# Optimization experiments

Hardware: AMD Instinct MI355X
Metric: run time of the kernel (lower is better)

Reference implementation:

```python
import jax, jax.numpy as jnp
import numpy as np

D_IN = 768
D_OUT = 768
NUM_HEADS = 12
HEAD_DIM = D_OUT // NUM_HEADS
SEQ = 4096
BATCH = 1


def setup_inputs() -> dict:
    key = jax.random.key(0)
    ks = jax.random.split(key, 6)
    s = 1.0 / np.sqrt(D_IN)
    return {
        "x": jax.random.normal(ks[0], (BATCH, SEQ, D_IN), dtype=jnp.float32),
        "W_query": jax.random.normal(ks[1], (D_IN, D_OUT), dtype=jnp.float32) * s,
        "W_key": jax.random.normal(ks[2], (D_IN, D_OUT), dtype=jnp.float32) * s,
        "W_value": jax.random.normal(ks[3], (D_IN, D_OUT), dtype=jnp.float32) * s,
        "W_out": jax.random.normal(ks[4], (D_OUT, D_OUT), dtype=jnp.float32) * s,
        "b_out": jax.random.normal(ks[5], (D_OUT,), dtype=jnp.float32) * 0.01,
    }


def reference(x, W_query, W_key, W_value, W_out, b_out):
    B, S, _ = x.shape
    # QKV projections (qkv_bias=False)
    q = (x @ W_query).reshape(B, S, NUM_HEADS, HEAD_DIM)
    k = (x @ W_key).reshape(B, S, NUM_HEADS, HEAD_DIM)
    v = (x @ W_value).reshape(B, S, NUM_HEADS, HEAD_DIM)
    # attention scores [B, H, S, S] with causal mask
    scores = jnp.einsum("bqhd,bkhd->bhqk", q, k) / jnp.sqrt(
        jnp.asarray(HEAD_DIM, dtype=x.dtype)
    )
    causal = jnp.tril(jnp.ones((S, S), dtype=bool))
    scores = jnp.where(causal, scores, jnp.finfo(x.dtype).min)
    attn = jax.nn.softmax(scores, axis=-1)  # dropout p=0.0 -> identity
    ctx = jnp.einsum("bhqk,bkhd->bqhd", attn, v).reshape(B, S, D_OUT)
    return ctx @ W_out + b_out
```

## Files before the change

### kernel.cpp

```cpp
#include <hip/hip_runtime.h>
#include <stdint.h>

#define SEQ 4096
#define DM 768
#define NH 12
#define HD 64

typedef __attribute__((ext_vector_type(8))) short bf8;
typedef __attribute__((ext_vector_type(4))) float f4;
typedef __attribute__((ext_vector_type(16))) float f32x16;

static __device__ __forceinline__ f4 mfma_bf16(bf8 a, bf8 b, f4 c) {
  return __builtin_amdgcn_mfma_f32_16x16x32_bf16(a, b, c, 0, 0, 0);
}
static __device__ __forceinline__ f32x16 mfma32(bf8 a, bf8 b, f32x16 c) {
  return __builtin_amdgcn_mfma_f32_32x32x16_bf16(a, b, c, 0, 0, 0);
}

static __device__ __forceinline__ unsigned short f2bf(float f) {
  unsigned int u = __float_as_uint(f);
  u += 0x7FFFu + ((u >> 16) & 1u);
  return (unsigned short)(u >> 16);
}

static __device__ __forceinline__ unsigned int cvtpk(float lo, float hi) {
  unsigned int r;
  asm("v_cvt_pk_bf16_f32 %0, %1, %2" : "=v"(r) : "v"(lo), "v"(hi));
  return r;
}

static __device__ __forceinline__ void gload_lds16(const void* g, void* l) {
  __builtin_amdgcn_global_load_lds(
      (const __attribute__((address_space(1))) void*)g,
      (__attribute__((address_space(3))) void*)l, 16, 0, 0);
}

__global__ __launch_bounds__(256) void k_cvt(const float* __restrict__ x,
                                             unsigned short* __restrict__ xb) {
  int i = (blockIdx.x * 256 + threadIdx.x) * 4;
  float4 v = *reinterpret_cast<const float4*>(x + i);
  ushort4 o;
  o.x = f2bf(v.x); o.y = f2bf(v.y); o.z = f2bf(v.z); o.w = f2bf(v.w);
  *reinterpret_cast<ushort4*>(xb + i) = o;
}

__global__ __launch_bounds__(256) void k_tw(const float* __restrict__ w0,
                                            const float* __restrict__ w1,
                                            const float* __restrict__ w2,
                                            const float* __restrict__ w3,
                                            unsigned short* __restrict__ wt) {
  const float* W = blockIdx.z == 0 ? w0 : blockIdx.z == 1 ? w1
                 : blockIdx.z == 2 ? w2 : w3;
  unsigned short* WT = wt + (size_t)blockIdx.z * DM * DM;
  __shared__ float t[32][33];
  int c0 = blockIdx.x * 32, r0 = blockIdx.y * 32;
  int lx = threadIdx.x & 31, ly = threadIdx.x >> 5;
#pragma unroll
  for (int rr = 0; rr < 32; rr += 8)
    t[ly + rr][lx] = W[(size_t)(r0 + ly + rr) * DM + c0 + lx];
  __syncthreads();
#pragma unroll
  for (int rr = 0; rr < 32; rr += 8)
    WT[(size_t)(c0 + ly + rr) * DM + r0 + lx] = f2bf(t[lx][ly + rr]);
}

template <int MODE>
__global__ __launch_bounds__(256) void k_gemm(const unsigned short* __restrict__ A,
                                              const unsigned short* __restrict__ Bt,
                                              void* __restrict__ Cout,
                                              const float* __restrict__ bias,
                                              float scale) {
  constexpr int K = DM;
  __shared__ unsigned short sA[128 * 32];
  __shared__ unsigned short sB[64 * 32];
  const int t = threadIdx.x, lane = t & 63, w = t >> 6;
  const int wr = w >> 1, wc = w & 1;
  const int c = lane & 15, g = lane >> 4;
  const int brow = blockIdx.x * 128, bcol = blockIdx.y * 64;
  f4 acc[4][2] = {};
  for (int k0 = 0; k0 < K; k0 += 32) {
#pragma unroll
    for (int i = 0; i < 2; ++i) {
      int slot = w * 2 + i;
      int chunk = slot * 64 + lane;
      int row = chunk >> 2;
      int sl = (chunk & 3) ^ ((row >> 1) & 3);
      gload_lds16(A + (size_t)(brow + row) * K + k0 + sl * 8, &sA[slot * 512]);
    }
    {
      int chunk = w * 64 + lane;
      int row = chunk >> 2;
      int sl = (chunk & 3) ^ ((row >> 1) & 3);
      gload_lds16(Bt + (size_t)(bcol + row) * K + k0 + sl * 8, &sB[w * 512]);
    }
    __syncthreads();
    bf8 af[4], bfr[2];
#pragma unroll
    for (int m = 0; m < 4; ++m) {
      int row = wr * 64 + m * 16 + c;
      int off = row * 64 + ((g * 16) ^ (((row >> 1) & 3) << 4));
      af[m] = *reinterpret_cast<const bf8*>(reinterpret_cast<const char*>(sA) + off);
    }
#pragma unroll
    for (int n = 0; n < 2; ++n) {
      int row = wc * 32 + n * 16 + c;
      int off = row * 64 + ((g * 16) ^ (((row >> 1) & 3) << 4));
      bfr[n] = *reinterpret_cast<const bf8*>(reinterpret_cast<const char*>(sB) + off);
    }
#pragma unroll
    for (int m = 0; m < 4; ++m)
#pragma unroll
      for (int n = 0; n < 2; ++n)
        acc[m][n] = mfma_bf16(af[m], bfr[n], acc[m][n]);
    __syncthreads();
  }
#pragma unroll
  for (int m = 0; m < 4; ++m) {
#pragma unroll
    for (int n = 0; n < 2; ++n) {
      int col = bcol + wc * 32 + n * 16 + c;
      int row0 = brow + wr * 64 + m * 16 + g * 4;
      if (MODE == 0) {
        unsigned short* C = (unsigned short*)Cout;
        int h = col >> 6, d = col & 63;
#pragma unroll
        for (int r = 0; r < 4; ++r)
          C[((size_t)h * SEQ + row0 + r) * 64 + d] = f2bf(acc[m][n][r] * scale);
      } else if (MODE == 1) {
        unsigned short* C = (unsigned short*)Cout;
        int h = col >> 6, d = col & 63;
        ushort4 p;
        p.x = f2bf(acc[m][n][0]); p.y = f2bf(acc[m][n][1]);
        p.z = f2bf(acc[m][n][2]); p.w = f2bf(acc[m][n][3]);
        *reinterpret_cast<ushort4*>(
            C + ((((size_t)h * 64 + (row0 >> 6)) * 64 + d) * 64 + (row0 & 63))) = p;
      } else {
        float* C = (float*)Cout;
#pragma unroll
        for (int r = 0; r < 4; ++r)
          C[(size_t)(row0 + r) * DM + col] = acc[m][n][r] + bias[col];
      }
    }
  }
}

#define PSWAP(a, b) asm volatile("v_permlane32_swap_b32 %0, %1" : "+v"(a), "+v"(b))
#define SGB() __builtin_amdgcn_sched_barrier(0)

#define STAGE8K(srcbase, tile, dst) do {                                      \
    const unsigned short* s_ = (srcbase) + (size_t)(tile) * 4096 + kLaneOff;  \
    _Pragma("unroll")                                                         \
    for (int j_ = 0; j_ < 8; ++j_)                                            \
      gload_lds16(s_ + j_ * 512, (dst) + j_ * 1024);                          \
  } while (0)

#define PBUILD(sv, pfx, pfy) do {                                             \
    float p0_ = __builtin_amdgcn_exp2f(sv[0] - mn_);                          \
    float p1_ = __builtin_amdgcn_exp2f(sv[1] - mn_);                          \
    float p2_ = __builtin_amdgcn_exp2f(sv[2] - mn_);                          \
    float p3_ = __builtin_amdgcn_exp2f(sv[3] - mn_);                          \
    float p4_ = __builtin_amdgcn_exp2f(sv[4] - mn_);                          \
    float p5_ = __builtin_amdgcn_exp2f(sv[5] - mn_);                          \
    float p6_ = __builtin_amdgcn_exp2f(sv[6] - mn_);                          \
    float p7_ = __builtin_amdgcn_exp2f(sv[7] - mn_);                          \
    unsigned int wa0_ = cvtpk(p0_, p1_), wa1_ = cvtpk(p2_, p3_);              \
    unsigned int wb0_ = cvtpk(p4_, p5_), wb1_ = cvtpk(p6_, p7_);              \
    ls_ += ((p0_ + p1_) + (p2_ + p3_)) + ((p4_ + p5_) + (p6_ + p7_));         \
    float q0_ = __builtin_amdgcn_exp2f(sv[8] - mn_);                          \
    float q1_ = __builtin_amdgcn_exp2f(sv[9] - mn_);                          \
    float q2_ = __builtin_amdgcn_exp2f(sv[10] - mn_);                         \
    float q3_ = __builtin_amdgcn_exp2f(sv[11] - mn_);                         \
    float q4_ = __builtin_amdgcn_exp2f(sv[12] - mn_);                         \
    float q5_ = __builtin_amdgcn_exp2f(sv[13] - mn_);                         \
    float q6_ = __builtin_amdgcn_exp2f(sv[14] - mn_);                         \
    float q7_ = __builtin_amdgcn_exp2f(sv[15] - mn_);                         \
    unsigned int wc0_ = cvtpk(q0_, q1_), wc1_ = cvtpk(q2_, q3_);              \
    unsigned int wd0_ = cvtpk(q4_, q5_), wd1_ = cvtpk(q6_, q7_);              \
    ls_ += ((q0_ + q1_) + (q2_ + q3_)) + ((q4_ + q5_) + (q6_ + q7_));         \
    PSWAP(wa0_, wb0_);                                                        \
    PSWAP(wa1_, wb1_);                                                        \
    PSWAP(wc0_, wd0_);                                                        \
    PSWAP(wc1_, wd1_);                                                        \
    uint4 u0_ = {wa0_, wa1_, wb0_, wb1_};                                     \
    uint4 u1_ = {wc0_, wc1_, wd0_, wd1_};                                     \
    pfx = *reinterpret_cast<bf8*>(&u0_);                                      \
    pfy = *reinterpret_cast<bf8*>(&u1_);                                      \
  } while (0)

#define FMAX8(v, i0) fmaxf(fmaxf(fmaxf(v[i0], v[i0+1]), fmaxf(v[i0+2], v[i0+3])), \
                           fmaxf(fmaxf(v[i0+4], v[i0+5]), fmaxf(v[i0+6], v[i0+7])))

#define XHALF_MAX(x) do {                                                     \
    float cp_ = (x);                                                          \
    asm volatile("" : "+v"(cp_));                                             \
    PSWAP((x), cp_);                                                          \
    (x) = fmaxf((x), cp_);                                                    \
  } while (0)
#define XHALF_ADD(x) do {                                                     \
    float cp_ = (x);                                                          \
    asm volatile("" : "+v"(cp_));                                             \
    PSWAP((x), cp_);                                                          \
    (x) = (x) + cp_;                                                          \
  } while (0)

#define STEP64(t, stage_) do {                                                \
    asm volatile("s_waitcnt vmcnt(0)" ::: "memory");                          \
    SGB();                                                                    \
    const int x0_ = ((hi) ^ xq) << 4;                                         \
    const int x1_ = ((2 + hi) ^ xq) << 4;                                     \
    const int x2_ = ((4 + hi) ^ xq) << 4;                                     \
    const int x3_ = ((6 + hi) ^ xq) << 4;                                     \
    const char* kr0_ = kbuf + ql * 128;                                       \
    const char* kr1_ = kbuf + (32 + ql) * 128;                                \
    bf8 ka0_ = *(const bf8*)(kr0_ + x0_);                                     \
    bf8 kb0_ = *(const bf8*)(kr1_ + x0_);                                     \
    bf8 ka1_ = *(const bf8*)(kr0_ + x1_);                                     \
    bf8 kb1_ = *(const bf8*)(kr1_ + x1_);                                     \
    bf8 ka2_ = *(const bf8*)(kr0_ + x2_);                                     \
    bf8 kb2_ = *(const bf8*)(kr1_ + x2_);                                     \
    bf8 ka3_ = *(const bf8*)(kr0_ + x3_);                                     \
    bf8 kb3_ = *(const bf8*)(kr1_ + x3_);                                     \
    SGB();                                                                    \
    asm volatile("s_waitcnt lgkmcnt(0)" ::: "memory");                        \
    SGB();                                                                    \
    if (stage_) STAGE8K(Khp, (t) + 4, kbuf);                                  \
    f32x16 s0_ = {}, s1_ = {};                                                \
    __builtin_amdgcn_s_setprio(1);                                            \
    s0_ = mfma32(ka0_, qf[0], s0_);  s1_ = mfma32(kb0_, qf[0], s1_);          \
    s0_ = mfma32(ka1_, qf[1], s0_);  s1_ = mfma32(kb1_, qf[1], s1_);          \
    s0_ = mfma32(ka2_, qf[2], s0_);  s1_ = mfma32(kb2_, qf[2], s1_);          \
    s0_ = mfma32(ka3_, qf[3], s0_);  s1_ = mfma32(kb3_, qf[3], s1_);          \
    __builtin_amdgcn_s_setprio(0);                                            \
    if ((t) == dt) {                                                          \
      _Pragma("unroll")                                                       \
      for (int r_ = 0; r_ < 16; ++r_) {                                       \
        int kr_ = (t) * 64 + (r_ & 3) + 8 * (r_ >> 2) + 4 * hi;               \
        s0_[r_] = (kr_ > qg) ? -1e30f : s0_[r_];                              \
        s1_[r_] = (kr_ + 32 > qg) ? -1e30f : s1_[r_];                         \
      }                                                                       \
    }                                                                         \
    float tm_ = fmaxf(fmaxf(FMAX8(s0_, 0), FMAX8(s0_, 8)),                    \
                      fmaxf(FMAX8(s1_, 0), FMAX8(s1_, 8)));                   \
    XHALF_MAX(tm_);                                                           \
    float mn_, al_;                                                           \
    if (__all(tm_ <= m + 8.f)) {                                              \
      mn_ = m;                                                                \
      al_ = 1.0f;                                                             \
    } else {                                                                  \
      mn_ = fmaxf(m, tm_);                                                    \
      al_ = __builtin_amdgcn_exp2f(m - mn_);                                  \
      m = mn_;                                                                \
      _Pragma("unroll")                                                       \
      for (int r_ = 0; r_ < 16; ++r_) { o0[r_] *= al_; o1[r_] *= al_; }       \
    }                                                                         \
    float ls_ = 0.f;                                                          \
    bf8 pfA0_, pfA1_, pfB0_, pfB1_;                                           \
    PBUILD(s0_, pfA0_, pfA1_);                                                \
    PBUILD(s1_, pfB0_, pfB1_);                                                \
    XHALF_ADD(ls_);                                                           \
    l = l * al_ + ls_;                                                        \
    const char* vr0_ = vbuf + ql * 128;                                       \
    const char* vr1_ = vbuf + (32 + ql) * 128;                                \
    bf8 va0_ = *(const bf8*)(vr0_ + x0_);                                     \
    bf8 va1_ = *(const bf8*)(vr0_ + x1_);                                     \
    bf8 va2_ = *(const bf8*)(vr0_ + x2_);                                     \
    bf8 va3_ = *(const bf8*)(vr0_ + x3_);                                     \
    bf8 vb0_ = *(const bf8*)(vr1_ + x0_);                                     \
    bf8 vb1_ = *(const bf8*)(vr1_ + x1_);                                     \
    bf8 vb2_ = *(const bf8*)(vr1_ + x2_);                                     \
    bf8 vb3_ = *(const bf8*)(vr1_ + x3_);                                     \
    SGB();                                                                    \
    asm volatile("s_waitcnt lgkmcnt(0)" ::: "memory");                        \
    SGB();                                                                    \
    if (stage_) STAGE8K(Vtp, (t) + 4, vbuf);                                  \
    __builtin_amdgcn_s_setprio(1);                                            \
    o0 = mfma32(va0_, pfA0_, o0);                                             \
    o0 = mfma32(va1_, pfA1_, o0);                                             \
    o0 = mfma32(va2_, pfB0_, o0);                                             \
    o0 = mfma32(va3_, pfB1_, o0);                                             \
    o1 = mfma32(vb0_, pfA0_, o1);                                             \
    o1 = mfma32(vb1_, pfA1_, o1);                                             \
    o1 = mfma32(vb2_, pfB0_, o1);                                             \
    o1 = mfma32(vb3_, pfB1_, o1);                                             \
    __builtin_amdgcn_s_setprio(0);                                            \
  } while (0)

__global__ __launch_bounds__(256, 2) void k_attn(const unsigned short* __restrict__ Qh,
                                                 const unsigned short* __restrict__ Kh,
                                                 const unsigned short* __restrict__ Vt,
                                                 unsigned short* __restrict__ ctx) {
  const int tid = threadIdx.x;
  const int lane = tid & 63;
  const int w = tid >> 6;
  const int ql = lane & 31, hi = lane >> 5;
  const int xq = ql & 7;

  const int L = (int)blockIdx.x;
  const int W = (L & 7) * 96 + (L >> 3);
  const int h = W >> 6;
  const int b = W & 63;

  __shared__ __align__(16) char smem[66560];
  char* kbuf = smem + w * 8192;
  char* vbuf = smem + 32768 + w * 8192;
  float* sO = (float*)smem;
  float* sM = (float*)(smem + 65536);
  float* sL = (float*)(smem + 66048);

  const unsigned short* Khp = Kh + (size_t)h * SEQ * 64;
  const unsigned short* Qhp = Qh + (size_t)h * SEQ * 64;
  const unsigned short* Vtp = Vt + (size_t)h * SEQ * 64;
  const int kLaneOff = (lane >> 3) * 64 + ((lane & 7) ^ (lane >> 3)) * 8;

  for (int ph = 0; ph < 2; ++ph) {
    const int qt = ph ? (127 - b) : b;
    const int qg = qt * 32 + ql;
    const int dt = qt >> 1;
    bf8 qf[4];
    {
      const unsigned short* qp = Qhp + (size_t)qg * 64 + hi * 8;
      qf[0] = *reinterpret_cast<const bf8*>(qp);
      qf[1] = *reinterpret_cast<const bf8*>(qp + 16);
      qf[2] = *reinterpret_cast<const bf8*>(qp + 32);
      qf[3] = *reinterpret_cast<const bf8*>(qp + 48);
    }
    f32x16 o0 = {}, o1 = {};
    float m = -1e30f, l = 0.f;

    const int nt = (dt >= w) ? ((dt - w) >> 2) + 1 : 0;
    if (nt > 0) {
      STAGE8K(Khp, w, kbuf);
      STAGE8K(Vtp, w, vbuf);
      for (int i = 0; i < nt; ++i) {
        const int t = w + 4 * i;
        STEP64(t, (i + 1 < nt));
      }
    }
    __syncthreads();

#pragma unroll
    for (int r = 0; r < 16; ++r) {
      int dr = (r & 3) + 8 * (r >> 2) + 4 * hi;
      sO[w * 2048 + dr * 32 + ql] = o0[r];
      sO[w * 2048 + (32 + dr) * 32 + ql] = o1[r];
    }
    if (hi == 0) { sM[w * 32 + ql] = m; sL[w * 32 + ql] = l; }
    __syncthreads();
    {
      const int q = tid & 31;
      const int dblk = tid >> 5;
      float m0 = sM[q], m1 = sM[32 + q], m2 = sM[64 + q], m3 = sM[96 + q];
      float mn = fmaxf(fmaxf(m0, m1), fmaxf(m2, m3));
      float a0 = __builtin_amdgcn_exp2f(m0 - mn);
      float a1 = __builtin_amdgcn_exp2f(m1 - mn);
      float a2 = __builtin_amdgcn_exp2f(m2 - mn);
      float a3 = __builtin_amdgcn_exp2f(m3 - mn);
      float inv = 1.f / (a0 * sL[q] + a1 * sL[32 + q] + a2 * sL[64 + q] + a3 * sL[96 + q]);
      a0 *= inv; a1 *= inv; a2 *= inv; a3 *= inv;
      unsigned short* cp = ctx + (size_t)(qt * 32 + q) * DM + h * HD + dblk * 8;
#pragma unroll
      for (int j = 0; j < 8; j += 2) {
        int d = dblk * 8 + j;
        float v0 = sO[d * 32 + q] * a0 + sO[2048 + d * 32 + q] * a1 +
                   sO[4096 + d * 32 + q] * a2 + sO[6144 + d * 32 + q] * a3;
        float v1 = sO[(d + 1) * 32 + q] * a0 + sO[2048 + (d + 1) * 32 + q] * a1 +
                   sO[4096 + (d + 1) * 32 + q] * a2 + sO[6144 + (d + 1) * 32 + q] * a3;
        *reinterpret_cast<unsigned int*>(cp + j) = cvtpk(v0, v1);
      }
    }
    __syncthreads();
  }
}

extern "C" void kernel_launch(void* const* d_in, const int* in_sizes, int n_in,
                              void* d_out, int out_size, void* d_ws, size_t ws_size,
                              hipStream_t stream) {
  const float* x  = (const float*)d_in[0];
  const float* Wq = (const float*)d_in[1];
  const float* Wk = (const float*)d_in[2];
  const float* Wv = (const float*)d_in[3];
  const float* Wo = (const float*)d_in[4];
  const float* bo = (const float*)d_in[5];

  unsigned short* xb = (unsigned short*)d_ws;
  unsigned short* wt = xb + (size_t)SEQ * DM;
  unsigned short* Qh = wt + (size_t)4 * DM * DM;
  unsigned short* Kh = Qh + (size_t)SEQ * DM;
  unsigned short* Vt = Kh + (size_t)SEQ * DM;
  unsigned short* cx = Vt + (size_t)SEQ * DM;

  const float qscale = 1.4426950408889634f / 8.0f;

  k_cvt<<<(SEQ * DM) / 1024, 256, 0, stream>>>(x, xb);
  k_tw<<<dim3(24, 24, 4), 256, 0, stream>>>(Wq, Wk, Wv, Wo, wt);
  dim3 gg(SEQ / 128, DM / 64);
  k_gemm<0><<<gg, 256, 0, stream>>>(xb, wt, Qh, nullptr, qscale);
  k_gemm<0><<<gg, 256, 0, stream>>>(xb, wt + (size_t)DM * DM, Kh, nullptr, 1.0f);
  k_gemm<1><<<gg, 256, 0, stream>>>(xb, wt + (size_t)2 * DM * DM, Vt, nullptr, 1.0f);
  k_attn<<<dim3(768), 256, 0, stream>>>(Qh, Kh, Vt, cx);
  k_gemm<2><<<gg, 256, 0, stream>>>(cx, wt + (size_t)3 * DM * DM, d_out, bo, 1.0f);
}
```

Before: 122.7 us.

## Fuse Q/K/V projections into one GEMM launch and widen tiles to 128x128

The three separate Q, K and V projection GEMMs are merged into a single launch over a concatenated 2304-column weight matrix. The epilogue routes each output column zone to the Q (scaled), K, or transposed-V layout. The tile width grows from 64 to 128 columns, so each block reuses its A tile across twice as many outputs. The output projection uses the same wider tile. This removes two launches and repeated reads of x, at the cost of more accumulator registers and fewer blocks for the output GEMM (192 vs 384).

Measured after the change: 120.1 us. 2.1% less time.

```diff
diff --git a/kernel.cpp b/kernel.cpp
--- a/kernel.cpp
+++ b/kernel.cpp
@@ -65,36 +65,40 @@
 }
 
 template <int MODE>
-__global__ __launch_bounds__(256) void k_gemm(const unsigned short* __restrict__ A,
-                                              const unsigned short* __restrict__ Bt,
-                                              void* __restrict__ Cout,
-                                              const float* __restrict__ bias,
-                                              float scale) {
-  constexpr int K = DM;
+__global__ __launch_bounds__(256) void k_gemm2(const unsigned short* __restrict__ A,
+                                               const unsigned short* __restrict__ Bt,
+                                               unsigned short* __restrict__ Qh,
+                                               unsigned short* __restrict__ Kh,
+                                               unsigned short* __restrict__ Vtl,
+                                               float* __restrict__ Cf,
+                                               const float* __restrict__ bias,
+                                               float qscale) {
   __shared__ unsigned short sA[128 * 32];
-  __shared__ unsigned short sB[64 * 32];
+  __shared__ unsigned short sB[128 * 32];
   const int t = threadIdx.x, lane = t & 63, w = t >> 6;
   const int wr = w >> 1, wc = w & 1;
   const int c = lane & 15, g = lane >> 4;
-  const int brow = blockIdx.x * 128, bcol = blockIdx.y * 64;
-  f4 acc[4][2] = {};
-  for (int k0 = 0; k0 < K; k0 += 32) {
+  const int brow = blockIdx.x * 128, bcol = blockIdx.y * 128;
+  f4 acc[4][4] = {};
+  for (int k0 = 0; k0 < DM; k0 += 32) {
 #pragma unroll
     for (int i = 0; i < 2; ++i) {
       int slot = w * 2 + i;
       int chunk = slot * 64 + lane;
       int row = chunk >> 2;
       int sl = (chunk & 3) ^ ((row >> 1) & 3);
-      gload_lds16(A + (size_t)(brow + row) * K + k0 + sl * 8, &sA[slot * 512]);
-    }
-    {
-      int chunk = w * 64 + lane;
+      gload_lds16(A + (size_t)(brow + row) * DM + k0 + sl * 8, &sA[slot * 512]);
+    }
+#pragma unroll
+    for (int i = 0; i < 2; ++i) {
+      int slot = w * 2 + i;
+      int chunk = slot * 64 + lane;
       int row = chunk >> 2;
       int sl = (chunk & 3) ^ ((row >> 1) & 3);
-      gload_lds16(Bt + (size_t)(bcol + row) * K + k0 + sl * 8, &sB[w * 512]);
+      gload_lds16(Bt + (size_t)(bcol + row) * DM + k0 + sl * 8, &sB[slot * 512]);
     }
     __syncthreads();
-    bf8 af[4], bfr[2];
+    bf8 af[4], bfr[4];
 #pragma unroll
     for (int m = 0; m < 4; ++m) {
       int row = wr * 64 + m * 16 + c;
@@ -102,43 +106,47 @@
       af[m] = *reinterpret_cast<const bf8*>(reinterpret_cast<const char*>(sA) + off);
     }
 #pragma unroll
-    for (int n = 0; n < 2; ++n) {
-      int row = wc * 32 + n * 16 + c;
+    for (int n = 0; n < 4; ++n) {
+      int row = wc * 64 + n * 16 + c;
       int off = row * 64 + ((g * 16) ^ (((row >> 1) & 3) << 4));
       bfr[n] = *reinterpret_cast<const bf8*>(reinterpret_cast<const char*>(sB) + off);
     }
 #pragma unroll
     for (int m = 0; m < 4; ++m)
 #pragma unroll
-      for (int n = 0; n < 2; ++n)
+      for (int n = 0; n < 4; ++n)
         acc[m][n] = mfma_bf16(af[m], bfr[n], acc[m][n]);
     __syncthreads();
   }
 #pragma unroll
   for (int m = 0; m < 4; ++m) {
 #pragma unroll
-    for (int n = 0; n < 2; ++n) {
-      int col = bcol + wc * 32 + n * 16 + c;
+    for (int n = 0; n < 4; ++n) {
+      int col = bcol + wc * 64 + n * 16 + c;
       int row0 = brow + wr * 64 + m * 16 + g * 4;
-      if (MODE == 0) {
-        unsigned short* C = (unsigned short*)Cout;
-        int h = col >> 6, d = col & 63;
+      if (MODE == 3) {
+        int zone = col / 768;
+        int ci = col - zone * 768;
+        int h = ci >> 6, d = ci & 63;
+        if (zone == 0) {
+#pragma unroll
+          for (int r = 0; r < 4; ++r)
+            Qh[((size_t)h * SEQ + row0 + r) * 64 + d] = f2bf(acc[m][n][r] * qscale);
+        } else if (zone == 1) {
+#pragma unroll
+          for (int r = 0; r < 4; ++r)
+            Kh[((size_t)h * SEQ + row0 + r) * 64 + d] = f2bf(acc[m][n][r]);
+        } else {
+          ushort4 p;
+          p.x = f2bf(acc[m][n][0]); p.y = f2bf(acc[m][n][1]);
+          p.z = f2bf(acc[m][n][2]); p.w = f2bf(acc[m][n][3]);
+          *reinterpret_cast<ushort4*>(
+              Vtl + ((((size_t)h * 64 + (row0 >> 6)) * 64 + d) * 64 + (row0 & 63))) = p;
+        }
+      } else {
 #pragma unroll
         for (int r = 0; r < 4; ++r)
-          C[((size_t)h * SEQ + row0 + r) * 64 + d] = f2bf(acc[m][n][r] * scale);
-      } else if (MODE == 1) {
-        unsigned short* C = (unsigned short*)Cout;
-        int h = col >> 6, d = col & 63;
-        ushort4 p;
-        p.x = f2bf(acc[m][n][0]); p.y = f2bf(acc[m][n][1]);
-        p.z = f2bf(acc[m][n][2]); p.w = f2bf(acc[m][n][3]);
-        *reinterpret_cast<ushort4*>(
-            C + ((((size_t)h * 64 + (row0 >> 6)) * 64 + d) * 64 + (row0 & 63))) = p;
-      } else {
-        float* C = (float*)Cout;
-#pragma unroll
-        for (int r = 0; r < 4; ++r)
-          C[(size_t)(row0 + r) * DM + col] = acc[m][n][r] + bias[col];
+          Cf[(size_t)(row0 + r) * DM + col] = acc[m][n][r] + bias[col];
       }
     }
   }
@@ -393,10 +401,10 @@
 
   k_cvt<<<(SEQ * DM) / 1024, 256, 0, stream>>>(x, xb);
   k_tw<<<dim3(24, 24, 4), 256, 0, stream>>>(Wq, Wk, Wv, Wo, wt);
-  dim3 gg(SEQ / 128, DM / 64);
-  k_gemm<0><<<gg, 256, 0, stream>>>(xb, wt, Qh, nullptr, qscale);
-  k_gemm<0><<<gg, 256, 0, stream>>>(xb, wt + (size_t)DM * DM, Kh, nullptr, 1.0f);
-  k_gemm<1><<<gg, 256, 0, stream>>>(xb, wt + (size_t)2 * DM * DM, Vt, nullptr, 1.0f);
+  k_gemm2<3><<<dim3(SEQ / 128, 2304 / 128), 256, 0, stream>>>(
+      xb, wt, Qh, Kh, Vt, nullptr, nullptr, qscale);
   k_attn<<<dim3(768), 256, 0, stream>>>(Qh, Kh, Vt, cx);
-  k_gemm<2><<<gg, 256, 0, stream>>>(cx, wt + (size_t)3 * DM * DM, d_out, bo, 1.0f);
-}
+  k_gemm2<2><<<dim3(SEQ / 128, DM / 128), 256, 0, stream>>>(
+      cx, wt + (size_t)3 * DM * DM, nullptr, nullptr, nullptr,
+      (float*)d_out, bo, 1.0f);
+}
```
